# Kernel tuning notes

Hardware: AMD Instinct MI355X
Metric: run time of the kernel (lower is better)

Reference implementation:

```python
import jax, jax.numpy as jnp
import numpy as np

H, HKV, D = 16, 4, 64
ROPE_BASE = 10000.0
EPS = 1e-6


def _rms_norm(x):
    return x * jax.lax.rsqrt(jnp.mean(x * x, axis=-1, keepdims=True) + EPS)


def _rope_cos_sin(T, dtype):
    inv_freq = 1.0 / (ROPE_BASE ** (jnp.arange(0, D, 2, dtype=jnp.float32) / D))  # [D/2]
    t = jnp.arange(T, dtype=jnp.float32)
    freqs = jnp.outer(t, inv_freq)  # [T, D/2]
    return jnp.cos(freqs)[None, :, None, :].astype(dtype), jnp.sin(freqs)[None, :, None, :].astype(dtype)


def _apply_rope(x, cos, sin):
    d = x.shape[-1] // 2
    x1, x2 = x[..., :d], x[..., d:]
    return jnp.concatenate([x1 * cos + x2 * sin, -x1 * sin + x2 * cos], axis=-1)


def setup_inputs() -> dict:
    key = jax.random.key(0)
    ks = jax.random.split(key, 6)
    B, T, dm = 1, 2048, 1024
    x = jax.random.normal(ks[0], (B, T, dm), dtype=jnp.float32)
    q_w = jax.random.normal(ks[1], (H * D, dm), dtype=jnp.float32) * 0.02
    k_w = jax.random.normal(ks[2], (HKV * D, dm), dtype=jnp.float32) * 0.02
    v_w = jax.random.normal(ks[3], (HKV * D, dm), dtype=jnp.float32) * 0.02
    o_w = jax.random.normal(ks[4], (dm, H * D), dtype=jnp.float32) * 0.02
    temp = jnp.ones((H,), dtype=jnp.float32) * np.sqrt(D)  # per-head temperature buffer
    curvature = jnp.asarray(1.0, dtype=jnp.float32)
    return {"x": x, "q_w": q_w, "k_w": k_w, "v_w": v_w, "o_w": o_w, "temp": temp, "curvature": curvature}


def reference(x, q_w, k_w, v_w, o_w, temp, curvature):
    B, T, dm = x.shape
    # projections
    q = (x @ q_w.T).reshape(B, T, H, D)
    k = (x @ k_w.T).reshape(B, T, HKV, D)
    v = (x @ v_w.T).reshape(B, T, HKV, D)
    q, k = _rms_norm(q), _rms_norm(k)
    cos, sin = _rope_cos_sin(T, q.dtype)
    q = _apply_rope(q, cos, sin)
    k = _apply_rope(k, cos, sin)
    # GQA: repeat kv heads
    rep = H // HKV
    k = jnp.repeat(k, rep, axis=2)  # [B,T,H,D]
    v = jnp.repeat(v, rep, axis=2)
    c = curvature
    # hyperboloid lift: time component x0 = sqrt(1/c + ||x||^2)
    q0 = jnp.sqrt(1.0 / c + jnp.sum(q * q, axis=-1))  # [B,T,H]
    k0 = jnp.sqrt(1.0 / c + jnp.sum(k * k, axis=-1))
    # Minkowski inner product <q,k>_L = q.k_spatial - q0*k0  -> [B,H,Tq,Tk]
    mink = jnp.einsum('bqhd,bkhd->bhqk', q, k) - q0.transpose(0, 2, 1)[..., :, None] * k0.transpose(0, 2, 1)[..., None, :]
    # Lorentz distance d = arccosh(clamp(-c*<q,k>_L, 1+eps)) / sqrt(c)
    dist = jnp.arccosh(jnp.maximum(-c * mink, 1.0 + 1e-5)) / jnp.sqrt(c)
    scores = -dist / temp[None, :, None, None]
    causal = jnp.tril(jnp.ones((T, T), dtype=bool))
    scores = jnp.where(causal[None, None], scores, -jnp.inf)
    w = jax.nn.softmax(scores, axis=-1)  # [B,H,Tq,Tk]
    attn = jnp.einsum('bhqk,bkhd->bqhd', w, v).reshape(B, T, H * D)
    out = attn @ o_w.T  # [B,T,dm]
    spatial_norm = jnp.mean(jnp.sqrt(jnp.sum(q * q, axis=-1)))
    return out, spatial_norm
```

## Files before the change

### kernel.cpp

```cpp
#include <hip/hip_runtime.h>
#include <hip/hip_bf16.h>

typedef __attribute__((ext_vector_type(8))) short short8;
typedef __attribute__((ext_vector_type(4))) short bf16x4;
typedef __attribute__((ext_vector_type(4))) float f32x4;

#define TT 2048
#define DM 1024
#define NH 16
#define NKV 4
#define HD 64

#define MFMA32(a,b,c) __builtin_amdgcn_mfma_f32_16x16x32_bf16(a,b,c,0,0,0)
#define MFMA16(a,b,c) __builtin_amdgcn_mfma_f32_16x16x16bf16_1k(a,b,c,0,0,0)

__device__ __forceinline__ unsigned short f2bf(float x){
  unsigned int u = __float_as_uint(x);
  u += 0x7fffu + ((u >> 16) & 1u);
  return (unsigned short)(u >> 16);
}
__device__ __forceinline__ unsigned int pkbf2(float x, float y){
  union { __hip_bfloat162 h; unsigned int u; } t;
  t.h = __float22bfloat162_rn(make_float2(x, y));
  return t.u;
}
__device__ __forceinline__ void gl_lds16(const unsigned short* g, unsigned short* l){
  __builtin_amdgcn_global_load_lds(
      (__attribute__((address_space(1))) void*)g,
      (__attribute__((address_space(3))) void*)l, 16, 0, 0);
}

__global__ __launch_bounds__(256) void convertw_kernel(
    const float* __restrict__ x,
    const float* __restrict__ qw, const float* __restrict__ kw,
    const float* __restrict__ vw, const float* __restrict__ ow,
    unsigned short* __restrict__ xb,
    unsigned short* __restrict__ wqkv, unsigned short* __restrict__ owb){
  long v = (long)blockIdx.x * 256 + threadIdx.x;
  const float* src; unsigned short* dst; long base;
  if      (v < 524288) { src = x;  dst = xb;             base = v; }
  else if (v < 786432) { src = qw; dst = wqkv;           base = v - 524288; }
  else if (v < 851968) { src = kw; dst = wqkv + 1048576; base = v - 786432; }
  else if (v < 917504) { src = vw; dst = wqkv + 1310720; base = v - 851968; }
  else                 { src = ow; dst = owb;            base = v - 917504; }
  f32x4 d = *(const f32x4*)(src + base * 4);
  uint2 pk = { pkbf2(d[0], d[1]), pkbf2(d[2], d[3]) };
  *(uint2*)(dst + base * 4) = pk;
}

__global__ __launch_bounds__(256) void gemm1_fused(
    const unsigned short* __restrict__ xb, const unsigned short* __restrict__ wqkv,
    unsigned short* __restrict__ qb, unsigned short* __restrict__ kb,
    unsigned short* __restrict__ vt,
    float* __restrict__ q0, float* __restrict__ k0,
    float* __restrict__ bpart, const float* __restrict__ curv){
  __shared__ __align__(16) unsigned short As[2 * 64 * 32];
  __shared__ __align__(16) unsigned short Bs[2 * 64 * 32];
  __shared__ float Ct[64 * 65];
  __shared__ float bsum;
  const int tid = threadIdx.x, lane = tid & 63, wave = tid >> 6;
  const int hIdx = blockIdx.x;
  const int bm = blockIdx.y * 64, bn = hIdx * 64;
  const int wm = (wave >> 1) * 32, wn = (wave & 1) * 32;
  const int ml = lane & 15, quad = lane >> 4;
  if (tid == 0) bsum = 0.f;
  f32x4 acc[2][2];
  const f32x4 z = {0.f, 0.f, 0.f, 0.f};
  acc[0][0] = z; acc[0][1] = z; acc[1][0] = z; acc[1][1] = z;

  const int srow = wave * 16 + (lane >> 2), scol = (lane & 3) * 8;
  const unsigned short* Ag = xb   + (long)(bm + srow) * 1024 + scol;
  const unsigned short* Bg = wqkv + (long)(bn + srow) * 1024 + scol;
  unsigned short* Al0 = As + wave * 512;
  unsigned short* Al1 = As + 2048 + wave * 512;
  unsigned short* Bl0 = Bs + wave * 512;
  unsigned short* Bl1 = Bs + 2048 + wave * 512;

  for (int kk = 0; kk < 1024; kk += 64){
    __syncthreads();
    gl_lds16(Ag + kk,      Al0);
    gl_lds16(Ag + kk + 32, Al1);
    gl_lds16(Bg + kk,      Bl0);
    gl_lds16(Bg + kk + 32, Bl1);
    __syncthreads();
#pragma unroll
    for (int half = 0; half < 2; half++){
      const unsigned short* Ah = As + half * 2048;
      const unsigned short* Bh = Bs + half * 2048;
      short8 a0f = *(const short8*)&Ah[(wm + ml) * 32 + quad * 8];
      short8 a1f = *(const short8*)&Ah[(wm + 16 + ml) * 32 + quad * 8];
      short8 b0f = *(const short8*)&Bh[(wn + ml) * 32 + quad * 8];
      short8 b1f = *(const short8*)&Bh[(wn + 16 + ml) * 32 + quad * 8];
      acc[0][0] = MFMA32(a0f, b0f, acc[0][0]);
      acc[0][1] = MFMA32(a0f, b1f, acc[0][1]);
      acc[1][0] = MFMA32(a1f, b0f, acc[1][0]);
      acc[1][1] = MFMA32(a1f, b1f, acc[1][1]);
    }
  }
  __syncthreads();
#pragma unroll
  for (int i = 0; i < 2; i++)
#pragma unroll
    for (int j = 0; j < 2; j++)
#pragma unroll
      for (int r = 0; r < 4; r++)
        Ct[(wm + i * 16 + quad * 4 + r) * 65 + wn + j * 16 + ml] = acc[i][j][r];
  __syncthreads();

  if (hIdx < 20){
    const bool isq = hIdx < 16;
    const int h = isq ? hIdx : hIdx - 16;
    const float c = curv[0];
    unsigned short* ob = isq ? qb : kb;
    float* o0 = isq ? q0 : k0;
#pragma unroll 1
    for (int rr = 0; rr < 16; rr++){
      const int row = wave * 16 + rr;
      const int t = bm + row;
      float val = Ct[row * 65 + lane];
      float ss = val * val;
#pragma unroll
      for (int off = 1; off < 64; off <<= 1) ss += __shfl_xor(ss, off);
      float scale = __builtin_amdgcn_rsqf(ss * (1.f / 64.f) + 1e-6f);
      float xn = val * scale;
      float other = __shfl_xor(xn, 32);
      int fi = lane & 31;
      float ang = (float)t * __builtin_amdgcn_exp2f((float)fi * (-13.287712379549449f / 32.f));
      float sn, cs; __sincosf(ang, &sn, &cs);
      float outv = (lane < 32) ? (xn * cs + other * sn) : (xn * cs - other * sn);
      ob[((long)h * TT + t) * 64 + lane] = f2bf(outv);
      if (lane == 0){
        float sq = ss * scale * scale;
        o0[h * TT + t] = __builtin_amdgcn_sqrtf(1.f / c + sq);
        if (isq) atomicAdd(&bsum, __builtin_amdgcn_sqrtf(sq));
      }
    }
  } else {
    const int hk = hIdx - 20;
    const int d = tid >> 2, tseg = (tid & 3) * 16;
    uint4 w0, w1;
    w0.x = pkbf2(Ct[(tseg + 0) * 65 + d], Ct[(tseg + 1) * 65 + d]);
    w0.y = pkbf2(Ct[(tseg + 2) * 65 + d], Ct[(tseg + 3) * 65 + d]);
    w0.z = pkbf2(Ct[(tseg + 4) * 65 + d], Ct[(tseg + 5) * 65 + d]);
    w0.w = pkbf2(Ct[(tseg + 6) * 65 + d], Ct[(tseg + 7) * 65 + d]);
    w1.x = pkbf2(Ct[(tseg + 8) * 65 + d], Ct[(tseg + 9) * 65 + d]);
    w1.y = pkbf2(Ct[(tseg +10) * 65 + d], Ct[(tseg +11) * 65 + d]);
    w1.z = pkbf2(Ct[(tseg +12) * 65 + d], Ct[(tseg +13) * 65 + d]);
    w1.w = pkbf2(Ct[(tseg +14) * 65 + d], Ct[(tseg +15) * 65 + d]);
    const int tile = (bm + tseg) >> 4;
    unsigned short* dst = vt + ((long)(hk * 128 + tile) * 64 + d) * 16;
    *(uint4*)dst = w0;
    *(uint4*)(dst + 8) = w1;
  }
  __syncthreads();
  if (tid == 0) bpart[blockIdx.y * 24 + hIdx] = bsum;
}

__global__ __launch_bounds__(256, 3) void attn_kernel(
    const unsigned short* __restrict__ qb_, const unsigned short* __restrict__ kb_,
    const unsigned short* __restrict__ vt_,
    const float* __restrict__ q0_, const float* __restrict__ k0_,
    const float* __restrict__ temp, const float* __restrict__ curv,
    unsigned short* __restrict__ attn_out,
    const float* __restrict__ bpart, float* __restrict__ out_scalar){
  __shared__ float lds[8 * 1104];
  const int tid = threadIdx.x, lane = tid & 63, wave = tid >> 6;
  const int qt  = 127 - (blockIdx.x >> 3);
  const int sub = blockIdx.x & 7;
  const int kvh = sub >> 1, hp = sub & 1;
  const int h0 = kvh * 4 + hp * 2, h1 = h0 + 1;
  const int i0 = qt * 16;
  const int ml = lane & 15, quad = lane >> 4;
  const float c = curv[0];
  const float rsc = __builtin_amdgcn_rsqf(c);
  const float fac0 = -rsc / temp[h0];
  const float fac1 = -rsc / temp[h1];
  const f32x4 z = {0.f, 0.f, 0.f, 0.f};
  const unsigned short* kh = kb_ + (long)kvh * TT * 64;
  const unsigned short* vh = vt_ + (long)kvh * 128 * 1024;
  const float* k0h = k0_ + kvh * TT;

  short8 qa0 = *(const short8*)&qb_[((long)h0 * TT + i0 + ml) * 64 + quad * 8];
  short8 qa1 = *(const short8*)&qb_[((long)h0 * TT + i0 + ml) * 64 + 32 + quad * 8];
  short8 qb0 = *(const short8*)&qb_[((long)h1 * TT + i0 + ml) * 64 + quad * 8];
  short8 qb1 = *(const short8*)&qb_[((long)h1 * TT + i0 + ml) * 64 + 32 + quad * 8];
  const float q0c0 = c * q0_[h0 * TT + i0 + ml];
  const float q0c1 = c * q0_[h1 * TT + i0 + ml];
  const int rowq = i0 + ml;

  f32x4 o0[4], o1[4];
#pragma unroll
  for (int dt = 0; dt < 4; dt++){ o0[dt] = z; o1[dt] = z; }
  float l0 = 0.f, l1 = 0.f;

  const int nt = (i0 + 47) >> 5;

#pragma unroll 1
  for (int t = wave; t < nt; t += 4){
    const int j0 = t << 5;
    const unsigned short* kp = kh + (long)j0 * 64;
    short8 ka0 = *(const short8*)(kp + ml * 64 + quad * 8);
    short8 ka1 = *(const short8*)(kp + ml * 64 + 32 + quad * 8);
    short8 kc0 = *(const short8*)(kp + (16 + ml) * 64 + quad * 8);
    short8 kc1 = *(const short8*)(kp + (16 + ml) * 64 + 32 + quad * 8);
    f32x4 k0a = *(const f32x4*)(k0h + j0 + quad * 4);
    f32x4 k0b = *(const f32x4*)(k0h + j0 + 16 + quad * 4);
    const unsigned short* vpa = vh + (long)(j0 >> 4) * 1024;
    bf16x4 vfa0 = *(const bf16x4*)(vpa + ( 0 + ml) * 16 + quad * 4);
    bf16x4 vfa1 = *(const bf16x4*)(vpa + (16 + ml) * 16 + quad * 4);
    bf16x4 vfa2 = *(const bf16x4*)(vpa + (32 + ml) * 16 + quad * 4);
    bf16x4 vfa3 = *(const bf16x4*)(vpa + (48 + ml) * 16 + quad * 4);
    bf16x4 vfb0 = *(const bf16x4*)(vpa + 1024 + ( 0 + ml) * 16 + quad * 4);
    bf16x4 vfb1 = *(const bf16x4*)(vpa + 1024 + (16 + ml) * 16 + quad * 4);
    bf16x4 vfb2 = *(const bf16x4*)(vpa + 1024 + (32 + ml) * 16 + quad * 4);
    bf16x4 vfb3 = *(const bf16x4*)(vpa + 1024 + (48 + ml) * 16 + quad * 4);

    const int keyb = j0 + quad * 4;
    const bool nm = (j0 + 31 > i0);
    {
      f32x4 s0 = z, s1 = z;
      s0 = MFMA32(ka0, qa0, s0);
      s0 = MFMA32(ka1, qa1, s0);
      s1 = MFMA32(kc0, qa0, s1);
      s1 = MFMA32(kc1, qa1, s1);
      float p0[4], p1[4];
#pragma unroll
      for (int r = 0; r < 4; r++){
        float argA = fmaxf(__builtin_fmaf(-c, s0[r], q0c0 * k0a[r]), 1.00001f);
        float wA   = argA + __builtin_amdgcn_sqrtf(__builtin_fmaf(argA, argA, -1.f));
        float pA   = __builtin_amdgcn_exp2f(fac0 * __builtin_amdgcn_logf(wA));
        float argB = fmaxf(__builtin_fmaf(-c, s1[r], q0c0 * k0b[r]), 1.00001f);
        float wB   = argB + __builtin_amdgcn_sqrtf(__builtin_fmaf(argB, argB, -1.f));
        float pB   = __builtin_amdgcn_exp2f(fac0 * __builtin_amdgcn_logf(wB));
        if (nm){
          if (keyb + r > rowq)      pA = 0.f;
          if (keyb + 16 + r > rowq) pB = 0.f;
        }
        p0[r] = pA; p1[r] = pB;
        l0 += pA + pB;
      }
      uint2 pua = { pkbf2(p0[0], p0[1]), pkbf2(p0[2], p0[3]) };
      uint2 pub = { pkbf2(p1[0], p1[1]), pkbf2(p1[2], p1[3]) };
      bf16x4 pfa = *(bf16x4*)&pua;
      bf16x4 pfb = *(bf16x4*)&pub;
      o0[0] = MFMA16(vfa0, pfa, o0[0]);
      o0[1] = MFMA16(vfa1, pfa, o0[1]);
      o0[2] = MFMA16(vfa2, pfa, o0[2]);
      o0[3] = MFMA16(vfa3, pfa, o0[3]);
      o0[0] = MFMA16(vfb0, pfb, o0[0]);
      o0[1] = MFMA16(vfb1, pfb, o0[1]);
      o0[2] = MFMA16(vfb2, pfb, o0[2]);
      o0[3] = MFMA16(vfb3, pfb, o0[3]);
    }
    {
      f32x4 s0 = z, s1 = z;
      s0 = MFMA32(ka0, qb0, s0);
      s0 = MFMA32(ka1, qb1, s0);
      s1 = MFMA32(kc0, qb0, s1);
      s1 = MFMA32(kc1, qb1, s1);
      float p0[4], p1[4];
#pragma unroll
      for (int r = 0; r < 4; r++){
        float argA = fmaxf(__builtin_fmaf(-c, s0[r], q0c1 * k0a[r]), 1.00001f);
        float wA   = argA + __builtin_amdgcn_sqrtf(__builtin_fmaf(argA, argA, -1.f));
        float pA   = __builtin_amdgcn_exp2f(fac1 * __builtin_amdgcn_logf(wA));
        float argB = fmaxf(__builtin_fmaf(-c, s1[r], q0c1 * k0b[r]), 1.00001f);
        float wB   = argB + __builtin_amdgcn_sqrtf(__builtin_fmaf(argB, argB, -1.f));
        float pB   = __builtin_amdgcn_exp2f(fac1 * __builtin_amdgcn_logf(wB));
        if (nm){
          if (keyb + r > rowq)      pA = 0.f;
          if (keyb + 16 + r > rowq) pB = 0.f;
        }
        p0[r] = pA; p1[r] = pB;
        l1 += pA + pB;
      }
      uint2 pua = { pkbf2(p0[0], p0[1]), pkbf2(p0[2], p0[3]) };
      uint2 pub = { pkbf2(p1[0], p1[1]), pkbf2(p1[2], p1[3]) };
      bf16x4 pfa = *(bf16x4*)&pua;
      bf16x4 pfb = *(bf16x4*)&pub;
      o1[0] = MFMA16(vfa0, pfa, o1[0]);
      o1[1] = MFMA16(vfa1, pfa, o1[1]);
      o1[2] = MFMA16(vfa2, pfa, o1[2]);
      o1[3] = MFMA16(vfa3, pfa, o1[3]);
      o1[0] = MFMA16(vfb0, pfb, o1[0]);
      o1[1] = MFMA16(vfb1, pfb, o1[1]);
      o1[2] = MFMA16(vfb2, pfb, o1[2]);
      o1[3] = MFMA16(vfb3, pfb, o1[3]);
    }
  }
  l0 += __shfl_xor(l0, 16); l0 += __shfl_xor(l0, 32);
  l1 += __shfl_xor(l1, 16); l1 += __shfl_xor(l1, 32);
  {
    float* w0 = lds + wave * 1104;
    float* w1 = lds + (4 + wave) * 1104;
#pragma unroll
    for (int dt = 0; dt < 4; dt++){
      *(f32x4*)&w0[ml * 68 + dt * 16 + quad * 4] = o0[dt];
      *(f32x4*)&w1[ml * 68 + dt * 16 + quad * 4] = o1[dt];
    }
    if (quad == 0){ w0[1088 + ml] = l0; w1[1088 + ml] = l1; }
  }
  __syncthreads();
  {
    const int row = tid >> 4, c0 = (tid & 15) * 4;
#pragma unroll 1
    for (int hb = 0; hb < 2; hb++){
      const float* base = lds + hb * 4 * 1104;
      float L = 0.f; f32x4 s = z;
#pragma unroll
      for (int w = 0; w < 4; w++){
        const float* rg = base + w * 1104;
        L += rg[1088 + row];
        f32x4 t2 = *(const f32x4*)&rg[row * 68 + c0];
        s[0] += t2[0]; s[1] += t2[1]; s[2] += t2[2]; s[3] += t2[3];
      }
      float invL = __builtin_amdgcn_rcpf(L);
      const int h = hb ? h1 : h0;
      uint2 o = { pkbf2(s[0] * invL, s[1] * invL), pkbf2(s[2] * invL, s[3] * invL) };
      *(uint2*)&attn_out[(long)(i0 + row) * 1024 + h * 64 + c0] = o;
    }
  }
  if (blockIdx.x == 0 && tid < 64){
    float s = 0.f;
    for (int i = lane; i < 768; i += 64) s += bpart[i];
#pragma unroll
    for (int off = 1; off < 64; off <<= 1) s += __shfl_xor(s, off);
    if (lane == 0) out_scalar[0] = s * (1.f / 32768.f);
  }
}

__global__ __launch_bounds__(256) void gemm2_kernel(
    const unsigned short* __restrict__ A, const unsigned short* __restrict__ B,
    float* __restrict__ C){
  __shared__ __align__(16) unsigned short As[2 * 64 * 32];
  __shared__ __align__(16) unsigned short Bs[2 * 64 * 32];
  const int tid = threadIdx.x, lane = tid & 63, wave = tid >> 6;
  const int bm = blockIdx.y * 64, bn = blockIdx.x * 64;
  const int wm = (wave >> 1) * 32, wn = (wave & 1) * 32;
  const int ml = lane & 15, quad = lane >> 4;
  f32x4 acc[2][2];
  const f32x4 z = {0.f, 0.f, 0.f, 0.f};
  acc[0][0] = z; acc[0][1] = z; acc[1][0] = z; acc[1][1] = z;

  const int srow = wave * 16 + (lane >> 2), scol = (lane & 3) * 8;
  const unsigned short* Ag = A + (long)(bm + srow) * 1024 + scol;
  const unsigned short* Bg = B + (long)(bn + srow) * 1024 + scol;
  unsigned short* Al0 = As + wave * 512;
  unsigned short* Al1 = As + 2048 + wave * 512;
  unsigned short* Bl0 = Bs + wave * 512;
  unsigned short* Bl1 = Bs + 2048 + wave * 512;

  for (int kk = 0; kk < 1024; kk += 64){
    __syncthreads();
    gl_lds16(Ag + kk,      Al0);
    gl_lds16(Ag + kk + 32, Al1);
    gl_lds16(Bg + kk,      Bl0);
    gl_lds16(Bg + kk + 32, Bl1);
    __syncthreads();
#pragma unroll
    for (int half = 0; half < 2; half++){
      const unsigned short* Ah = As + half * 2048;
      const unsigned short* Bh = Bs + half * 2048;
      short8 a0f = *(const short8*)&Ah[(wm + ml) * 32 + quad * 8];
      short8 a1f = *(const short8*)&Ah[(wm + 16 + ml) * 32 + quad * 8];
      short8 b0f = *(const short8*)&Bh[(wn + ml) * 32 + quad * 8];
      short8 b1f = *(const short8*)&Bh[(wn + 16 + ml) * 32 + quad * 8];
      acc[0][0] = MFMA32(a0f, b0f, acc[0][0]);
      acc[0][1] = MFMA32(a0f, b1f, acc[0][1]);
      acc[1][0] = MFMA32(a1f, b0f, acc[1][0]);
      acc[1][1] = MFMA32(a1f, b1f, acc[1][1]);
    }
  }
#pragma unroll
  for (int i = 0; i < 2; i++)
#pragma unroll
    for (int j = 0; j < 2; j++)
#pragma unroll
      for (int r = 0; r < 4; r++)
        C[(long)(bm + wm + i * 16 + quad * 4 + r) * 1024 + bn + wn + j * 16 + ml] = acc[i][j][r];
}

extern "C" void kernel_launch(void* const* d_in, const int* in_sizes, int n_in,
                              void* d_out, int out_size, void* d_ws, size_t ws_size,
                              hipStream_t stream){
  const float* x    = (const float*)d_in[0];
  const float* qw   = (const float*)d_in[1];
  const float* kw   = (const float*)d_in[2];
  const float* vw   = (const float*)d_in[3];
  const float* ow   = (const float*)d_in[4];
  const float* temp = (const float*)d_in[5];
  const float* curv = (const float*)d_in[6];
  float* out = (float*)d_out;

  char* ws = (char*)d_ws;
  size_t off = 0;
  auto alloc = [&](size_t bytes) -> char* {
    char* p = ws + off;
    off += (bytes + 255) & ~(size_t)255;
    return p;
  };
  unsigned short* xb   = (unsigned short*)alloc((size_t)TT * DM * 2);
  unsigned short* wqkv = (unsigned short*)alloc((size_t)1536 * DM * 2);
  unsigned short* owb  = (unsigned short*)alloc((size_t)DM * DM * 2);
  unsigned short* qb   = (unsigned short*)alloc((size_t)NH * TT * HD * 2);
  unsigned short* kb   = (unsigned short*)alloc((size_t)NKV * TT * HD * 2);
  unsigned short* vt   = (unsigned short*)alloc((size_t)NKV * TT * HD * 2);
  float*          q0   = (float*)alloc((size_t)NH * TT * 4);
  float*          k0   = (float*)alloc((size_t)NKV * TT * 4);
  unsigned short* attn = (unsigned short*)alloc((size_t)TT * DM * 2);
  float*          bpart= (float*)alloc((size_t)768 * 4);

  convertw_kernel<<<4608, 256, 0, stream>>>(x, qw, kw, vw, ow, xb, wqkv, owb);
  gemm1_fused<<<dim3(24, 32), 256, 0, stream>>>(xb, wqkv, qb, kb, vt, q0, k0, bpart, curv);
  attn_kernel<<<1024, 256, 0, stream>>>(qb, kb, vt, q0, k0, temp, curv, attn,
                                        bpart, out + (size_t)TT * DM);
  gemm2_kernel<<<dim3(16, 32), 256, 0, stream>>>(attn, owb, out);
}
```

Measured before the change: 145.2 us.

## Double-buffer LDS tiles in both projection GEMMs to overlap loads with MFMA

Both GEMM kernels now keep two LDS buffers per operand and issue the global-to-LDS copy for the next K tile before computing on the current one, with one barrier per step instead of two. The goal is to hide global load latency behind MFMA work. In gemm1 the epilogue scratch Ct is aliased onto the A/B staging memory so total LDS stays about the same. The risk is extra LDS per block in gemm2, which may lower occupancy, and reliance on the async copy having completed by the barrier.

```diff
diff --git a/kernel.cpp b/kernel.cpp
--- a/kernel.cpp
+++ b/kernel.cpp
@@ -54,10 +54,11 @@
     unsigned short* __restrict__ vt,
     float* __restrict__ q0, float* __restrict__ k0,
     float* __restrict__ bpart, const float* __restrict__ curv){
-  __shared__ __align__(16) unsigned short As[2 * 64 * 32];
-  __shared__ __align__(16) unsigned short Bs[2 * 64 * 32];
-  __shared__ float Ct[64 * 65];
+  __shared__ __align__(16) unsigned short AB[2 * 8192];
   __shared__ float bsum;
+  unsigned short* As = AB;
+  unsigned short* Bs = AB + 8192;
+  float* Ct = (float*)AB;
   const int tid = threadIdx.x, lane = tid & 63, wave = tid >> 6;
   const int hIdx = blockIdx.x;
   const int bm = blockIdx.y * 64, bn = hIdx * 64;
@@ -71,33 +72,45 @@
   const int srow = wave * 16 + (lane >> 2), scol = (lane & 3) * 8;
   const unsigned short* Ag = xb   + (long)(bm + srow) * 1024 + scol;
   const unsigned short* Bg = wqkv + (long)(bn + srow) * 1024 + scol;
-  unsigned short* Al0 = As + wave * 512;
-  unsigned short* Al1 = As + 2048 + wave * 512;
-  unsigned short* Bl0 = Bs + wave * 512;
-  unsigned short* Bl1 = Bs + 2048 + wave * 512;
-
-  for (int kk = 0; kk < 1024; kk += 64){
+
+#define G1_STAGE(nb, ko)                                           \
+  do {                                                             \
+    gl_lds16(Ag + (ko),      As + (nb) * 4096 + wave * 512);       \
+    gl_lds16(Ag + (ko) + 32, As + (nb) * 4096 + 2048 + wave * 512);\
+    gl_lds16(Bg + (ko),      Bs + (nb) * 4096 + wave * 512);       \
+    gl_lds16(Bg + (ko) + 32, Bs + (nb) * 4096 + 2048 + wave * 512);\
+  } while (0)
+
+#define G1_COMPUTE(b)                                                   \
+  do {                                                                  \
+    _Pragma("unroll")                                                   \
+    for (int half = 0; half < 2; half++){                               \
+      const unsigned short* Ah = As + (b) * 4096 + half * 2048;         \
+      const unsigned short* Bh = Bs + (b) * 4096 + half * 2048;         \
+      short8 a0f = *(const short8*)&Ah[(wm + ml) * 32 + quad * 8];      \
+      short8 a1f = *(const short8*)&Ah[(wm + 16 + ml) * 32 + quad * 8]; \
+      short8 b0f = *(const short8*)&Bh[(wn + ml) * 32 + quad * 8];      \
+      short8 b1f = *(const short8*)&Bh[(wn + 16 + ml) * 32 + quad * 8]; \
+      acc[0][0] = MFMA32(a0f, b0f, acc[0][0]);                          \
+      acc[0][1] = MFMA32(a0f, b1f, acc[0][1]);                          \
+      acc[1][0] = MFMA32(a1f, b0f, acc[1][0]);                          \
+      acc[1][1] = MFMA32(a1f, b1f, acc[1][1]);                          \
+    }                                                                   \
+  } while (0)
+
+  G1_STAGE(0, 0);
+  __syncthreads();
+  for (int kk = 0; kk < 1024; kk += 128){
+    G1_STAGE(1, kk + 64);
+    G1_COMPUTE(0);
     __syncthreads();
-    gl_lds16(Ag + kk,      Al0);
-    gl_lds16(Ag + kk + 32, Al1);
-    gl_lds16(Bg + kk,      Bl0);
-    gl_lds16(Bg + kk + 32, Bl1);
+    if (kk + 128 < 1024) G1_STAGE(0, kk + 128);
+    G1_COMPUTE(1);
     __syncthreads();
-#pragma unroll
-    for (int half = 0; half < 2; half++){
-      const unsigned short* Ah = As + half * 2048;
-      const unsigned short* Bh = Bs + half * 2048;
-      short8 a0f = *(const short8*)&Ah[(wm + ml) * 32 + quad * 8];
-      short8 a1f = *(const short8*)&Ah[(wm + 16 + ml) * 32 + quad * 8];
-      short8 b0f = *(const short8*)&Bh[(wn + ml) * 32 + quad * 8];
-      short8 b1f = *(const short8*)&Bh[(wn + 16 + ml) * 32 + quad * 8];
-      acc[0][0] = MFMA32(a0f, b0f, acc[0][0]);
-      acc[0][1] = MFMA32(a0f, b1f, acc[0][1]);
-      acc[1][0] = MFMA32(a1f, b0f, acc[1][0]);
-      acc[1][1] = MFMA32(a1f, b1f, acc[1][1]);
-    }
-  }
-  __syncthreads();
+  }
+#undef G1_STAGE
+#undef G1_COMPUTE
+
 #pragma unroll
   for (int i = 0; i < 2; i++)
 #pragma unroll
@@ -332,8 +345,8 @@
 __global__ __launch_bounds__(256) void gemm2_kernel(
     const unsigned short* __restrict__ A, const unsigned short* __restrict__ B,
     float* __restrict__ C){
-  __shared__ __align__(16) unsigned short As[2 * 64 * 32];
-  __shared__ __align__(16) unsigned short Bs[2 * 64 * 32];
+  __shared__ __align__(16) unsigned short As[2 * 4096];
+  __shared__ __align__(16) unsigned short Bs[2 * 4096];
   const int tid = threadIdx.x, lane = tid & 63, wave = tid >> 6;
   const int bm = blockIdx.y * 64, bn = blockIdx.x * 64;
   const int wm = (wave >> 1) * 32, wn = (wave & 1) * 32;
@@ -345,32 +358,45 @@
   const int srow = wave * 16 + (lane >> 2), scol = (lane & 3) * 8;
   const unsigned short* Ag = A + (long)(bm + srow) * 1024 + scol;
   const unsigned short* Bg = B + (long)(bn + srow) * 1024 + scol;
-  unsigned short* Al0 = As + wave * 512;
-  unsigned short* Al1 = As + 2048 + wave * 512;
-  unsigned short* Bl0 = Bs + wave * 512;
-  unsigned short* Bl1 = Bs + 2048 + wave * 512;
-
-  for (int kk = 0; kk < 1024; kk += 64){
+
+#define G2_STAGE(nb, ko)                                           \
+  do {                                                             \
+    gl_lds16(Ag + (ko),      As + (nb) * 4096 + wave * 512);       \
+    gl_lds16(Ag + (ko) + 32, As + (nb) * 4096 + 2048 + wave * 512);\
+    gl_lds16(Bg + (ko),      Bs + (nb) * 4096 + wave * 512);       \
+    gl_lds16(Bg + (ko) + 32, Bs + (nb) * 4096 + 2048 + wave * 512);\
+  } while (0)
+
+#define G2_COMPUTE(b)                                                   \
+  do {                                                                  \
+    _Pragma("unroll")                                                   \
+    for (int half = 0; half < 2; half++){                               \
+      const unsigned short* Ah = As + (b) * 4096 + half * 2048;         \
+      const unsigned short* Bh = Bs + (b) * 4096 + half * 2048;         \
+      short8 a0f = *(const short8*)&Ah[(wm + ml) * 32 + quad * 8];      \
+      short8 a1f = *(const short8*)&Ah[(wm + 16 + ml) * 32 + quad * 8]; \
+      short8 b0f = *(const short8*)&Bh[(wn + ml) * 32 + quad * 8];      \
+      short8 b1f = *(const short8*)&Bh[(wn + 16 + ml) * 32 + quad * 8]; \
+      acc[0][0] = MFMA32(a0f, b0f, acc[0][0]);                          \
+      acc[0][1] = MFMA32(a0f, b1f, acc[0][1]);                          \
+      acc[1][0] = MFMA32(a1f, b0f, acc[1][0]);                          \
+      acc[1][1] = MFMA32(a1f, b1f, acc[1][1]);                          \
+    }                                                                   \
+  } while (0)
+
+  G2_STAGE(0, 0);
+  __syncthreads();
+  for (int kk = 0; kk < 1024; kk += 128){
+    G2_STAGE(1, kk + 64);
+    G2_COMPUTE(0);
     __syncthreads();
-    gl_lds16(Ag + kk,      Al0);
-    gl_lds16(Ag + kk + 32, Al1);
-    gl_lds16(Bg + kk,      Bl0);
-    gl_lds16(Bg + kk + 32, Bl1);
+    if (kk + 128 < 1024) G2_STAGE(0, kk + 128);
+    G2_COMPUTE(1);
     __syncthreads();
-#pragma unroll
-    for (int half = 0; half < 2; half++){
-      const unsigned short* Ah = As + half * 2048;
-      const unsigned short* Bh = Bs + half * 2048;
-      short8 a0f = *(const short8*)&Ah[(wm + ml) * 32 + quad * 8];
-      short8 a1f = *(const short8*)&Ah[(wm + 16 + ml) * 32 + quad * 8];
-      short8 b0f = *(const short8*)&Bh[(wn + ml) * 32 + quad * 8];
-      short8 b1f = *(const short8*)&Bh[(wn + 16 + ml) * 32 + quad * 8];
-      acc[0][0] = MFMA32(a0f, b0f, acc[0][0]);
-      acc[0][1] = MFMA32(a0f, b1f, acc[0][1]);
-      acc[1][0] = MFMA32(a1f, b0f, acc[1][0]);
-      acc[1][1] = MFMA32(a1f, b1f, acc[1][1]);
-    }
-  }
+  }
+#undef G2_STAGE
+#undef G2_COMPUTE
+
 #pragma unroll
   for (int i = 0; i < 2; i++)
 #pragma unroll
```

New measurement: 147.6 us. About the same (+1.7%).
